# Kernel optimization log

Measured on AMD Instinct MI355X. Metric: run time of the kernel, lower is better.

The kernel has to match this reference:

```python
import jax, jax.numpy as jnp
import numpy as np

N, K = 300000, 27          # active voxels, 3x3x3 kernel offsets
C_IN, C_MID, C_S, C_OUT = 256, 128, 32, 8
BN_EPS = 1e-5


def setup_inputs() -> dict:
    key = jax.random.key(0)
    ks = jax.random.split(key, 8)
    x = jax.random.normal(ks[0], (N, C_IN), jnp.float32)
    nbr_idx = jax.random.randint(ks[1], (N, K), 0, N, dtype=jnp.int32)
    nbr_mask = jax.random.bernoulli(ks[2], 0.5, (N, K))
    W1 = jax.random.normal(ks[3], (K, C_IN, C_MID), jnp.float32) * (1.0 / np.sqrt(K * C_IN))
    gamma1 = jnp.ones((C_MID,), jnp.float32)
    beta1 = jnp.zeros((C_MID,), jnp.float32)
    W2 = jax.random.normal(ks[4], (C_MID, C_S), jnp.float32) * (1.0 / np.sqrt(C_MID))
    gamma2 = jnp.ones((C_S,), jnp.float32)
    beta2 = jnp.zeros((C_S,), jnp.float32)
    W3 = jax.random.normal(ks[5], (C_S, C_OUT), jnp.float32) * (1.0 / np.sqrt(C_S))
    return {"x": x, "nbr_idx": nbr_idx, "nbr_mask": nbr_mask, "W1": W1,
            "gamma1": gamma1, "beta1": beta1, "W2": W2, "gamma2": gamma2,
            "beta2": beta2, "W3": W3}


def _batch_norm(h, gamma, beta):
    # training-mode BN over active points (Minkowski BN normalizes over N)
    mean = jnp.mean(h, axis=0)
    var = jnp.mean(jnp.square(h - mean), axis=0)
    return (h - mean) * jax.lax.rsqrt(var + BN_EPS) * gamma + beta


def _sparse_conv3(x, nbr_idx, mask_f, W1):
    # gather-GEMM-scatter over the 27 kernel offsets; fixed small loop over K
    out = jnp.zeros((x.shape[0], W1.shape[-1]), x.dtype)
    for k in range(K):
        gathered = x[nbr_idx[:, k]] * mask_f[:, k, None]  # [N, C_in]
        out = out + gathered @ W1[k]                      # [N, C_mid]
    return out


def reference(x, nbr_idx, nbr_mask, W1, gamma1, beta1, W2, gamma2, beta2, W3):
    mask_f = nbr_mask.astype(x.dtype)
    # enc1: 3x3x3 sparse conv -> BN -> ReLU
    h = _sparse_conv3(x, nbr_idx, mask_f, W1)
    h = jax.nn.relu(_batch_norm(h, gamma1, beta1))
    # reg head: 1x1 conv (dense linear on features) -> BN -> 1x1 conv
    h = _batch_norm(h @ W2, gamma2, beta2)
    return h @ W3  # [N, 8]
```

## Files before the change

kernel.cpp:

```cpp
#include <hip/hip_runtime.h>
#include <hip/hip_bf16.h>

#define NPTS  300000
#define KOFF  27
#define CIN   256
#define CMID  128
#define CS    32
#define COUT  8
#define BN_EPS 1e-5f

typedef __bf16 bf16x8 __attribute__((ext_vector_type(8)));
typedef float  f32x4  __attribute__((ext_vector_type(4)));

__device__ __forceinline__ float bf2f(unsigned short u){
  return __uint_as_float(((unsigned int)u) << 16);
}
__device__ __forceinline__ float bf2f_lo(unsigned int w){
  return __uint_as_float(w << 16);
}
__device__ __forceinline__ float bf2f_hi(unsigned int w){
  return __uint_as_float(w & 0xffff0000u);
}
__device__ __forceinline__ unsigned short f2bf(float f){
  unsigned int x = __float_as_uint(f);
  return (unsigned short)((x + 0x7fffu + ((x >> 16) & 1u)) >> 16);
}

__global__ void detect_mask_kernel(const unsigned int* __restrict__ mask,
                                   int* __restrict__ flag){
  __shared__ int cnt;
  const int t = threadIdx.x;
  if (t == 0) cnt = 0;
  __syncthreads();
  int local = 0;
  for (int i = t; i < 2048; i += 256){
    unsigned int v = mask[i];
    local += (v <= 1u) ? 1 : 0;
  }
  atomicAdd(&cnt, local);
  __syncthreads();
  if (t == 0) *flag = (cnt > 1843) ? 0 : ((cnt > 512) ? 2 : 1);
}

__global__ __launch_bounds__(256)
void cvt_x_kernel(const float* __restrict__ x, unsigned int* __restrict__ xb4){
  const unsigned int total = NPTS * CIN / 8;
  for (unsigned int j = blockIdx.x * 256 + threadIdx.x; j < total; j += gridDim.x * 256){
    const float4* s = reinterpret_cast<const float4*>(x) + (size_t)j * 2;
    float4 a = s[0], b = s[1];
    uint4 o;
    o.x = (unsigned)f2bf(a.x) | ((unsigned)f2bf(a.y) << 16);
    o.y = (unsigned)f2bf(a.z) | ((unsigned)f2bf(a.w) << 16);
    o.z = (unsigned)f2bf(b.x) | ((unsigned)f2bf(b.y) << 16);
    o.w = (unsigned)f2bf(b.z) | ((unsigned)f2bf(b.w) << 16);
    reinterpret_cast<uint4*>(xb4)[j] = o;
  }
}

__global__ __launch_bounds__(256)
void cvt_w1t_kernel(const float* __restrict__ W1, unsigned short* __restrict__ w1t){
  __shared__ float ls[64][133];
  const int t = threadIdx.x;
  const int k = blockIdx.x >> 2, ib = blockIdx.x & 3;
  const float* src = W1 + (size_t)k * (CIN * CMID) + (size_t)ib * 64 * CMID;
  for (int e = t; e < 64 * 128; e += 256){
    int i = e >> 7, c = e & 127;
    ls[i][c] = src[e];
  }
  __syncthreads();
  unsigned short* dst = w1t + (size_t)k * (CMID * CIN) + ib * 64;
  for (int e = t; e < 64 * 128; e += 256){
    int i = e & 63, c = e >> 6;
    dst[(size_t)c * CIN + i] = f2bf(ls[i][c]);
  }
}

__global__ __launch_bounds__(256)
void conv1_mfma_kernel(const unsigned short* __restrict__ xb,
                       const int* __restrict__ nbr,
                       const void* __restrict__ maskp,
                       const unsigned short* __restrict__ W1T,
                       const int* __restrict__ flagp,
                       unsigned short* __restrict__ h1t)
{
  __shared__ __align__(16) char xs[64 * 512];
  __shared__ int   ni[64][KOFF];
  __shared__ float mf[64][KOFF];

  const int t = threadIdx.x;
  const int pbase = blockIdx.x * 64;
  const int flag = *flagp;

  for (int e = t; e < 64 * KOFF; e += 256){
    int r = e / KOFF, k = e - r * KOFF;
    int p = pbase + r;
    float m = 0.f; int idx = 0;
    if (p < NPTS){
      int g = p * KOFF + k;
      idx = nbr[g];
      if (flag == 0)      m = (float)(((const int*)maskp)[g]);
      else if (flag == 1) m = (float)(((const unsigned char*)maskp)[g]);
      else                m = ((const float*)maskp)[g];
    }
    ni[r][k] = idx; mf[r][k] = m;
  }

  f32x4 acc[2][4];
  #pragma unroll
  for (int mm = 0; mm < 2; mm++)
    #pragma unroll
    for (int n = 0; n < 4; n++)
      acc[mm][n] = (f32x4){0.f, 0.f, 0.f, 0.f};

  const int lane = t & 63;
  const int wave = t >> 6;
  const int wr = wave >> 1;
  const int wc = wave & 1;
  const int l15 = lane & 15;
  const int l4  = lane >> 4;

  const int sr  = t >> 2;
  const int sc0 = t & 3;

  __syncthreads();

  for (int k = 0; k < KOFF; ++k){
    {
      const float m = mf[sr][k];
      const unsigned short* src = xb + (size_t)ni[sr][k] * CIN;
      #pragma unroll
      for (int q = 0; q < 8; ++q){
        const int c = sc0 + q * 4;
        uint4 v = make_uint4(0u, 0u, 0u, 0u);
        if (m != 0.f) v = *reinterpret_cast<const uint4*>(src + c * 8);
        const int dst = sr * 512 + ((c * 16) ^ ((sr & 7) << 4));
        *reinterpret_cast<uint4*>(xs + dst) = v;
      }
    }
    __syncthreads();

    const unsigned short* wk = W1T + (size_t)k * (CMID * CIN);
    #pragma unroll
    for (int kk = 0; kk < 8; ++kk){
      bf16x8 b[4];
      #pragma unroll
      for (int n = 0; n < 4; ++n){
        const int col = wc * 64 + n * 16 + l15;
        b[n] = *reinterpret_cast<const bf16x8*>(wk + (size_t)col * CIN + kk * 32 + l4 * 8);
      }
      #pragma unroll
      for (int mm = 0; mm < 2; ++mm){
        const int row = wr * 32 + mm * 16 + l15;
        const int off = row * 512 + ((kk * 64 + l4 * 16) ^ ((row & 7) << 4));
        bf16x8 a = *reinterpret_cast<const bf16x8*>(xs + off);
        #pragma unroll
        for (int n = 0; n < 4; ++n)
          acc[mm][n] = __builtin_amdgcn_mfma_f32_16x16x32_bf16(a, b[n], acc[mm][n], 0, 0, 0);
      }
    }
    __syncthreads();
  }

  #pragma unroll
  for (int mm = 0; mm < 2; ++mm){
    const int row = pbase + wr * 32 + mm * 16 + l4 * 4;
    if (row + 3 < NPTS){
      #pragma unroll
      for (int n = 0; n < 4; ++n){
        const int col = wc * 64 + n * 16 + l15;
        ushort4 o;
        o.x = f2bf(acc[mm][n][0]);
        o.y = f2bf(acc[mm][n][1]);
        o.z = f2bf(acc[mm][n][2]);
        o.w = f2bf(acc[mm][n][3]);
        *reinterpret_cast<ushort4*>(h1t + (size_t)col * NPTS + row) = o;
      }
    }
  }
}

__global__ __launch_bounds__(256)
void stats1_kernel(const unsigned short* __restrict__ h1t, float* __restrict__ stats1){
  const int c = blockIdx.x;
  const int t = threadIdx.x;
  const uint4* p = reinterpret_cast<const uint4*>(h1t + (size_t)c * NPTS);
  float s = 0.f, s2 = 0.f;
  for (int i = t; i < NPTS / 8; i += 256){
    uint4 v = p[i];
    float f0 = bf2f_lo(v.x), f1 = bf2f_hi(v.x);
    float f2 = bf2f_lo(v.y), f3 = bf2f_hi(v.y);
    float f4 = bf2f_lo(v.z), f5 = bf2f_hi(v.z);
    float f6 = bf2f_lo(v.w), f7 = bf2f_hi(v.w);
    s  += ((f0 + f1) + (f2 + f3)) + ((f4 + f5) + (f6 + f7));
    s2 += ((f0*f0 + f1*f1) + (f2*f2 + f3*f3)) + ((f4*f4 + f5*f5) + (f6*f6 + f7*f7));
  }
  #pragma unroll
  for (int o = 32; o > 0; o >>= 1){
    s  += __shfl_xor(s, o);
    s2 += __shfl_xor(s2, o);
  }
  __shared__ float rs[4], rs2[4];
  const int wave = t >> 6;
  if ((t & 63) == 0){ rs[wave] = s; rs2[wave] = s2; }
  __syncthreads();
  if (t == 0){
    stats1[c]        = rs[0] + rs[1] + rs[2] + rs[3];
    stats1[CMID + c] = rs2[0] + rs2[1] + rs2[2] + rs2[3];
  }
}

__global__ __launch_bounds__(256)
void bn1_gemm2_kernel(const unsigned short* __restrict__ h1t, const float* __restrict__ stats1,
                      const float* __restrict__ gamma1, const float* __restrict__ beta1,
                      const float* __restrict__ W2, float* __restrict__ h2)
{
  __shared__ float hs[64][129];
  __shared__ float w2s[128][36];
  __shared__ float scl[CMID], sft[CMID];
  const int t = threadIdx.x;
  const int pbase = blockIdx.x * 64;

  if (t < CMID){
    const float inv = 1.f / (float)NPTS;
    float mean = stats1[t] * inv;
    float var  = stats1[CMID + t] * inv - mean * mean;
    float rs = rsqrtf(var + BN_EPS);
    float sc = gamma1[t] * rs;
    scl[t] = sc; sft[t] = beta1[t] - mean * sc;
  }
  for (int e = t; e < CMID * CS; e += 256)
    w2s[e >> 5][e & 31] = W2[e];
  __syncthreads();

  {
    const int p = t & 63;
    const int gp = pbase + p;
    #pragma unroll
    for (int cc = 0; cc < 32; ++cc){
      const int c = (t >> 6) + cc * 4;
      float v = 0.f;
      if (gp < NPTS) v = bf2f(h1t[(size_t)c * NPTS + gp]);
      hs[p][c] = fmaxf(v * scl[c] + sft[c], 0.f);
    }
  }
  __syncthreads();

  const int cp = t >> 2;
  const int c0 = (t & 3) * 8;
  float a0=0,a1=0,a2=0,a3=0,a4=0,a5=0,a6=0,a7=0;
  #pragma unroll 8
  for (int i = 0; i < CMID; ++i){
    const float hv = hs[cp][i];
    const float4 wa = *reinterpret_cast<const float4*>(&w2s[i][c0]);
    const float4 wb = *reinterpret_cast<const float4*>(&w2s[i][c0 + 4]);
    a0 = fmaf(hv, wa.x, a0); a1 = fmaf(hv, wa.y, a1);
    a2 = fmaf(hv, wa.z, a2); a3 = fmaf(hv, wa.w, a3);
    a4 = fmaf(hv, wb.x, a4); a5 = fmaf(hv, wb.y, a5);
    a6 = fmaf(hv, wb.z, a6); a7 = fmaf(hv, wb.w, a7);
  }
  if (pbase + cp < NPTS){
    float* o = h2 + (size_t)(pbase + cp) * CS + c0;
    *reinterpret_cast<float4*>(o)     = make_float4(a0, a1, a2, a3);
    *reinterpret_cast<float4*>(o + 4) = make_float4(a4, a5, a6, a7);
  }
}

__global__ void stats_f32_kernel(const float* __restrict__ h,
                                 float* __restrict__ out)
{
  const int t = threadIdx.x;
  const int c = t & 31;
  const int rsub = t >> 5;
  float s = 0.f, s2 = 0.f;
  for (size_t r = (size_t)blockIdx.x * 8 + rsub; r < NPTS; r += (size_t)gridDim.x * 8){
    float v = h[r * CS + c];
    s += v; s2 += v * v;
  }
  __shared__ float red[256];
  red[t] = s; __syncthreads();
  if (t < 32){
    float tot = 0.f;
    #pragma unroll
    for (int u = 0; u < 8; u++) tot += red[u * 32 + t];
    atomicAdd(&out[c], tot);
  }
  __syncthreads();
  red[t] = s2; __syncthreads();
  if (t < 32){
    float tot = 0.f;
    #pragma unroll
    for (int u = 0; u < 8; u++) tot += red[u * 32 + t];
    atomicAdd(&out[CS + c], tot);
  }
}

__global__ __launch_bounds__(256)
void bn2_gemm3_kernel(const float* __restrict__ h2, const float* __restrict__ stats2,
                      const float* __restrict__ gamma2, const float* __restrict__ beta2,
                      const float* __restrict__ W3, float* __restrict__ out)
{
  __shared__ float w3s[CS][COUT];
  __shared__ float hs[32][36];
  __shared__ float scl[CS], sft[CS];
  const int t = threadIdx.x;
  if (t < CS){
    const float inv = 1.f / (float)NPTS;
    float mean = stats2[t] * inv;
    float var  = stats2[CS + t] * inv - mean * mean;
    float rs = rsqrtf(var + BN_EPS);
    float sc = gamma2[t] * rs;
    scl[t] = sc; sft[t] = beta2[t] - mean * sc;
  }
  if (t < CS * COUT) w3s[t / COUT][t % COUT] = W3[t];
  __syncthreads();

  const int pblock = blockIdx.x * 32;
  const int r = t >> 3, c4 = (t & 7) * 4;
  {
    float4 v = *reinterpret_cast<const float4*>(h2 + (size_t)(pblock + r) * CS + c4);
    v.x = v.x * scl[c4+0] + sft[c4+0];
    v.y = v.y * scl[c4+1] + sft[c4+1];
    v.z = v.z * scl[c4+2] + sft[c4+2];
    v.w = v.w * scl[c4+3] + sft[c4+3];
    *reinterpret_cast<float4*>(&hs[r][c4]) = v;
  }
  __syncthreads();
  const int pp = t >> 3, c = t & 7;
  float a = 0.f;
  #pragma unroll
  for (int i = 0; i < CS; i++) a += hs[pp][i] * w3s[i][c];
  out[(size_t)(pblock + pp) * COUT + c] = a;
}

extern "C" void kernel_launch(void* const* d_in, const int* in_sizes, int n_in,
                              void* d_out, int out_size, void* d_ws, size_t ws_size,
                              hipStream_t stream) {
  const float* x    = (const float*)d_in[0];
  const int*   nbr  = (const int*)d_in[1];
  const void*  mask = d_in[2];
  const float* W1   = (const float*)d_in[3];
  const float* g1   = (const float*)d_in[4];
  const float* b1   = (const float*)d_in[5];
  const float* W2   = (const float*)d_in[6];
  const float* g2   = (const float*)d_in[7];
  const float* b2   = (const float*)d_in[8];
  const float* W3   = (const float*)d_in[9];
  float* out = (float*)d_out;

  char* ws = (char*)d_ws;
  int*   flag   = (int*)ws;
  float* stats1 = (float*)(ws + 256);
  float* stats2 = (float*)(ws + 1280);
  unsigned short* h1t = (unsigned short*)(ws + 4096);
  unsigned short* xb  = (unsigned short*)(ws + 4096 + 76800000ull);
  unsigned short* w1t = (unsigned short*)(ws + 4096 + 230400000ull);
  float*          h2  = (float*)(ws + 4096 + 232169472ull);

  hipMemsetAsync(ws, 0, 4096, stream);
  detect_mask_kernel<<<1, 256, 0, stream>>>((const unsigned int*)mask, flag);
  cvt_x_kernel<<<2048, 256, 0, stream>>>(x, (unsigned int*)xb);
  cvt_w1t_kernel<<<KOFF * 4, 256, 0, stream>>>(W1, w1t);
  conv1_mfma_kernel<<<(NPTS + 63) / 64, 256, 0, stream>>>(xb, nbr, mask, w1t, flag, h1t);
  stats1_kernel<<<CMID, 256, 0, stream>>>(h1t, stats1);
  bn1_gemm2_kernel<<<(NPTS + 63) / 64, 256, 0, stream>>>(h1t, stats1, g1, b1, W2, h2);
  stats_f32_kernel<<<512, 256, 0, stream>>>(h2, stats2);
  bn2_gemm3_kernel<<<NPTS / 32, 256, 0, stream>>>(h2, stats2, g2, b2, W3, out);
}
```

Baseline: 2.681 ms.

## Double-buffer conv1 gather via async global_load_lds and prefetch W1 into registers

The conv1 kernel now gathers neighbor rows straight into LDS with global_load_lds, using two LDS buffers so the gather for offset k+1 runs while MFMAs consume offset k. Masked neighbors are redirected to a zeroed workspace row instead of being branched on, and all W1 fragments for an offset are loaded into registers before the MFMA loop. The bn1_gemm2 load of h1t is also changed to read two bf16 values per 32-bit load. In exchange, LDS and register use go up and launch_bounds asks for 2 blocks per CU, so occupancy or register spilling may suffer.

Result: faster. 2.597 ms (-3.1%).

```diff
diff --git a/kernel.cpp b/kernel.cpp
--- a/kernel.cpp
+++ b/kernel.cpp
@@ -24,6 +24,12 @@
 __device__ __forceinline__ unsigned short f2bf(float f){
   unsigned int x = __float_as_uint(f);
   return (unsigned short)((x + 0x7fffu + ((x >> 16) & 1u)) >> 16);
+}
+
+__device__ __forceinline__ void gload_lds16(const void* g, void* l){
+  __builtin_amdgcn_global_load_lds(
+      (const __attribute__((address_space(1))) unsigned int*)g,
+      (__attribute__((address_space(3))) unsigned int*)l, 16, 0, 0);
 }
 
 __global__ void detect_mask_kernel(const unsigned int* __restrict__ mask,
@@ -75,17 +81,36 @@
   }
 }
 
-__global__ __launch_bounds__(256)
+__device__ __forceinline__ void stage_tile(char* xsbuf, const int (*ni)[KOFF],
+                                           const unsigned short* __restrict__ xb,
+                                           const unsigned short* __restrict__ zp,
+                                           int wave, int lane, int k)
+{
+  const int half  = lane >> 5;
+  const int cphys = lane & 31;
+  #pragma unroll
+  for (int i = 0; i < 8; ++i){
+    const int r0 = wave * 16 + i * 2;
+    const int r  = r0 + half;
+    const int idxv = ni[r][k];
+    const int clog = cphys ^ (r & 7);
+    const unsigned short* src = (idxv < 0) ? (zp + clog * 8)
+                                           : (xb + (size_t)idxv * CIN + clog * 8);
+    gload_lds16(src, xsbuf + r0 * 512);
+  }
+}
+
+__global__ __launch_bounds__(256, 2)
 void conv1_mfma_kernel(const unsigned short* __restrict__ xb,
                        const int* __restrict__ nbr,
                        const void* __restrict__ maskp,
                        const unsigned short* __restrict__ W1T,
                        const int* __restrict__ flagp,
+                       const unsigned short* __restrict__ zp,
                        unsigned short* __restrict__ h1t)
 {
-  __shared__ __align__(16) char xs[64 * 512];
-  __shared__ int   ni[64][KOFF];
-  __shared__ float mf[64][KOFF];
+  __shared__ __align__(16) char xs[2][64 * 512];
+  __shared__ int ni[64][KOFF];
 
   const int t = threadIdx.x;
   const int pbase = blockIdx.x * 64;
@@ -94,23 +119,17 @@
   for (int e = t; e < 64 * KOFF; e += 256){
     int r = e / KOFF, k = e - r * KOFF;
     int p = pbase + r;
-    float m = 0.f; int idx = 0;
+    int v = -1;
     if (p < NPTS){
       int g = p * KOFF + k;
-      idx = nbr[g];
+      float m;
       if (flag == 0)      m = (float)(((const int*)maskp)[g]);
       else if (flag == 1) m = (float)(((const unsigned char*)maskp)[g]);
       else                m = ((const float*)maskp)[g];
+      if (m != 0.f) v = nbr[g];
     }
-    ni[r][k] = idx; mf[r][k] = m;
-  }
-
-  f32x4 acc[2][4];
-  #pragma unroll
-  for (int mm = 0; mm < 2; mm++)
-    #pragma unroll
-    for (int n = 0; n < 4; n++)
-      acc[mm][n] = (f32x4){0.f, 0.f, 0.f, 0.f};
+    ni[r][k] = v;
+  }
 
   const int lane = t & 63;
   const int wave = t >> 6;
@@ -119,45 +138,45 @@
   const int l15 = lane & 15;
   const int l4  = lane >> 4;
 
-  const int sr  = t >> 2;
-  const int sc0 = t & 3;
-
+  f32x4 acc[2][4];
+  #pragma unroll
+  for (int mm = 0; mm < 2; mm++)
+    #pragma unroll
+    for (int n = 0; n < 4; n++)
+      acc[mm][n] = (f32x4){0.f, 0.f, 0.f, 0.f};
+
+  __syncthreads();
+  stage_tile(xs[0], ni, xb, zp, wave, lane, 0);
   __syncthreads();
 
   for (int k = 0; k < KOFF; ++k){
-    {
-      const float m = mf[sr][k];
-      const unsigned short* src = xb + (size_t)ni[sr][k] * CIN;
-      #pragma unroll
-      for (int q = 0; q < 8; ++q){
-        const int c = sc0 + q * 4;
-        uint4 v = make_uint4(0u, 0u, 0u, 0u);
-        if (m != 0.f) v = *reinterpret_cast<const uint4*>(src + c * 8);
-        const int dst = sr * 512 + ((c * 16) ^ ((sr & 7) << 4));
-        *reinterpret_cast<uint4*>(xs + dst) = v;
-      }
-    }
-    __syncthreads();
-
+    const int cur = k & 1;
+
+    bf16x8 breg[8][4];
     const unsigned short* wk = W1T + (size_t)k * (CMID * CIN);
     #pragma unroll
-    for (int kk = 0; kk < 8; ++kk){
-      bf16x8 b[4];
+    for (int kk = 0; kk < 8; ++kk)
       #pragma unroll
       for (int n = 0; n < 4; ++n){
         const int col = wc * 64 + n * 16 + l15;
-        b[n] = *reinterpret_cast<const bf16x8*>(wk + (size_t)col * CIN + kk * 32 + l4 * 8);
+        breg[kk][n] = *reinterpret_cast<const bf16x8*>(wk + (size_t)col * CIN + kk * 32 + l4 * 8);
       }
+
+    if (k + 1 < KOFF) stage_tile(xs[cur ^ 1], ni, xb, zp, wave, lane, k + 1);
+
+    #pragma unroll
+    for (int kk = 0; kk < 8; ++kk){
       #pragma unroll
       for (int mm = 0; mm < 2; ++mm){
         const int row = wr * 32 + mm * 16 + l15;
         const int off = row * 512 + ((kk * 64 + l4 * 16) ^ ((row & 7) << 4));
-        bf16x8 a = *reinterpret_cast<const bf16x8*>(xs + off);
+        bf16x8 a = *reinterpret_cast<const bf16x8*>(xs[cur] + off);
         #pragma unroll
         for (int n = 0; n < 4; ++n)
-          acc[mm][n] = __builtin_amdgcn_mfma_f32_16x16x32_bf16(a, b[n], acc[mm][n], 0, 0, 0);
+          acc[mm][n] = __builtin_amdgcn_mfma_f32_16x16x32_bf16(a, breg[kk][n], acc[mm][n], 0, 0, 0);
       }
     }
+
     __syncthreads();
   }
 
@@ -233,14 +252,18 @@
   __syncthreads();
 
   {
-    const int p = t & 63;
-    const int gp = pbase + p;
-    #pragma unroll
-    for (int cc = 0; cc < 32; ++cc){
-      const int c = (t >> 6) + cc * 4;
-      float v = 0.f;
-      if (gp < NPTS) v = bf2f(h1t[(size_t)c * NPTS + gp]);
-      hs[p][c] = fmaxf(v * scl[c] + sft[c], 0.f);
+    const int tp = t & 31;
+    const int cg = t >> 5;
+    const int p0 = 2 * tp;
+    #pragma unroll
+    for (int cc = 0; cc < 16; ++cc){
+      const int c = cg + cc * 8;
+      unsigned int v = 0;
+      if (pbase + p0 < NPTS)
+        v = *reinterpret_cast<const unsigned int*>(h1t + (size_t)c * NPTS + pbase + p0);
+      float flo = bf2f_lo(v), fhi = bf2f_hi(v);
+      hs[p0][c]     = fmaxf(flo * scl[c] + sft[c], 0.f);
+      hs[p0 + 1][c] = fmaxf(fhi * scl[c] + sft[c], 0.f);
     }
   }
   __syncthreads();
@@ -349,8 +372,9 @@
 
   char* ws = (char*)d_ws;
   int*   flag   = (int*)ws;
-  float* stats1 = (float*)(ws + 256);
-  float* stats2 = (float*)(ws + 1280);
+  unsigned short* zp = (unsigned short*)(ws + 1024);
+  float* stats1 = (float*)(ws + 2048);
+  float* stats2 = (float*)(ws + 3072);
   unsigned short* h1t = (unsigned short*)(ws + 4096);
   unsigned short* xb  = (unsigned short*)(ws + 4096 + 76800000ull);
   unsigned short* w1t = (unsigned short*)(ws + 4096 + 230400000ull);
@@ -360,7 +384,7 @@
   detect_mask_kernel<<<1, 256, 0, stream>>>((const unsigned int*)mask, flag);
   cvt_x_kernel<<<2048, 256, 0, stream>>>(x, (unsigned int*)xb);
   cvt_w1t_kernel<<<KOFF * 4, 256, 0, stream>>>(W1, w1t);
-  conv1_mfma_kernel<<<(NPTS + 63) / 64, 256, 0, stream>>>(xb, nbr, mask, w1t, flag, h1t);
+  conv1_mfma_kernel<<<(NPTS + 63) / 64, 256, 0, stream>>>(xb, nbr, mask, w1t, flag, zp, h1t);
   stats1_kernel<<<CMID, 256, 0, stream>>>(h1t, stats1);
   bn1_gemm2_kernel<<<(NPTS + 63) / 64, 256, 0, stream>>>(h1t, stats1, g1, b1, W2, h2);
   stats_f32_kernel<<<512, 256, 0, stream>>>(h2, stats2);
```
